# Optimization experiments

Hardware: AMD Instinct MI355X
Metric: run time of the kernel (lower is better)

Reference implementation:

```python
import jax, jax.numpy as jnp
import numpy as np

V = 50000

def _spmm(edge_vals, edge_row, edge_col, x):
    # sparse (V,V) @ dense (V,F) via gather + segment_sum
    return jax.ops.segment_sum(edge_vals[:, None] * x[edge_col], edge_row, num_segments=V)

def setup_inputs() -> dict:
    key = jax.random.key(0)
    ks = jax.random.split(key, 6)
    B, Cin, Cout, K, E = 4, 128, 128, 4, 800000
    x = jax.random.normal(ks[0], (B, Cin, V), dtype=jnp.float32)
    edge_row = jax.random.randint(ks[1], (E,), 0, V, dtype=jnp.int32)
    edge_col = jax.random.randint(ks[2], (E,), 0, V, dtype=jnp.int32)
    edge_vals = jax.random.normal(ks[3], (E,), dtype=jnp.float32) * 0.05
    std = np.sqrt(2.0 / (Cin * K)).astype(np.float32)
    weights = jax.random.normal(ks[4], (K, Cin, Cout), dtype=jnp.float32) * std
    biases = jnp.full((Cout,), 0.01, dtype=jnp.float32)
    return {"x": x, "edge_row": edge_row, "edge_col": edge_col,
            "edge_vals": edge_vals, "weights": weights, "biases": biases}

def reference(x, edge_row, edge_col, edge_vals, weights, biases):
    B, Cin, Vv = x.shape
    K = weights.shape[0]
    # (B,Cin,V) -> (V, B*Cin)
    x0 = jnp.transpose(x, (2, 0, 1)).reshape(Vv, B * Cin)
    xs = [x0]
    if K > 1:
        x1 = _spmm(edge_vals, edge_row, edge_col, x0)
        xs.append(x1)
        for _ in range(2, K):
            x2 = 2.0 * _spmm(edge_vals, edge_row, edge_col, x1) - x0
            xs.append(x2)
            x0, x1 = x1, x2
    xk = jnp.stack(xs, 0).reshape(K, Vv, B, Cin)
    # tensordot over (K, Cin): (K,V,B,Cin) x (K,Cin,Cout) -> (V,B,Cout)
    out = jnp.einsum('kvbc,kco->vbo', xk, weights)
    out = out + biases
    # permute (V,B,Cout) -> (B,Cout,V)
    return jnp.transpose(out, (1, 2, 0))
```

## Files before the change

### kernel.cpp

```cpp
#include <hip/hip_runtime.h>

#define V_N   50000
#define B_N   4
#define C_IN  128
#define C_OUT 128
#define E_N   800000
#define F_N   512
#define M_TOT 200000

#define SCAN_BLK  1024
#define SCAN_NB   ((V_N + SCAN_BLK - 1) / SCAN_BLK)

typedef unsigned short ushort_t;
typedef __attribute__((ext_vector_type(8))) short short8;
typedef __attribute__((ext_vector_type(4))) float f32x4;

#define AS1 __attribute__((address_space(1)))
#define AS3 __attribute__((address_space(3)))
__device__ __forceinline__ void gl_lds16(const void* gp, void* lp) {
    __builtin_amdgcn_global_load_lds((const AS1 unsigned int*)gp,
                                     (AS3 unsigned int*)lp, 16, 0, 0);
}

__device__ __forceinline__ float bf_lo(unsigned u) { return __uint_as_float(u << 16); }
__device__ __forceinline__ float bf_hi(unsigned u) { return __uint_as_float(u & 0xFFFF0000u); }
__device__ __forceinline__ ushort_t f2bf(float f) {
    unsigned u = __float_as_uint(f);
    u += 0x7FFFu + ((u >> 16) & 1u);
    return (ushort_t)(u >> 16);
}

__global__ __launch_bounds__(256) void k_transpose_in(const float* __restrict__ x,
                                                      ushort_t* __restrict__ x0) {
    __shared__ float tile[32][33];
    int vb = blockIdx.x * 32;
    int fb = blockIdx.y * 32;
    int tx = threadIdx.x, ty = threadIdx.y;
#pragma unroll
    for (int i = 0; i < 32; i += 8) {
        int f = fb + ty + i, v = vb + tx;
        float val = 0.f;
        if (v < V_N) val = x[(size_t)f * V_N + v];
        tile[ty + i][tx] = val;
    }
    __syncthreads();
#pragma unroll
    for (int i = 0; i < 32; i += 8) {
        int v = vb + ty + i, f = fb + tx;
        if (v < V_N) x0[(size_t)v * F_N + f] = f2bf(tile[tx][ty + i]);
    }
}

__global__ __launch_bounds__(256) void k_hist(const int* __restrict__ row,
                                              int* __restrict__ counts) {
    int e = blockIdx.x * blockDim.x + threadIdx.x;
    if (e < E_N) atomicAdd(&counts[row[e]], 1);
}

__global__ __launch_bounds__(256) void k_scan_blk(const int* __restrict__ counts,
                                                  int* __restrict__ row_ptr,
                                                  int* __restrict__ blk_sums) {
    __shared__ int s[256];
    int t = threadIdx.x;
    int base = blockIdx.x * SCAN_BLK + t * 4;
    int c0 = (base + 0 < V_N) ? counts[base + 0] : 0;
    int c1 = (base + 1 < V_N) ? counts[base + 1] : 0;
    int c2 = (base + 2 < V_N) ? counts[base + 2] : 0;
    int c3 = (base + 3 < V_N) ? counts[base + 3] : 0;
    int p1 = c0, p2 = c0 + c1, p3 = c0 + c1 + c2, tot = p3 + c3;
    s[t] = tot;
    __syncthreads();
#pragma unroll
    for (int off = 1; off < 256; off <<= 1) {
        int v = (t >= off) ? s[t - off] : 0;
        __syncthreads();
        s[t] += v;
        __syncthreads();
    }
    int excl = (t == 0) ? 0 : s[t - 1];
    if (base + 0 < V_N) row_ptr[base + 0] = excl;
    if (base + 1 < V_N) row_ptr[base + 1] = excl + p1;
    if (base + 2 < V_N) row_ptr[base + 2] = excl + p2;
    if (base + 3 < V_N) row_ptr[base + 3] = excl + p3;
    if (t == 255) blk_sums[blockIdx.x] = s[255];
}

__global__ __launch_bounds__(64) void k_scan_top(const int* __restrict__ blk_sums,
                                                 int* __restrict__ blk_off) {
    int t = threadIdx.x;
    int v = (t < SCAN_NB) ? blk_sums[t] : 0;
#pragma unroll
    for (int off = 1; off < 64; off <<= 1) {
        int u = __shfl_up(v, off);
        if (t >= off) v += u;
    }
    blk_off[t] = v;
}

__global__ __launch_bounds__(256) void k_scan_add(const int* __restrict__ blk_off,
                                                  int* __restrict__ row_ptr,
                                                  int* __restrict__ next) {
    int b = blockIdx.x, t = threadIdx.x;
    int off = (b == 0) ? 0 : blk_off[b - 1];
    int base = b * SCAN_BLK + t * 4;
#pragma unroll
    for (int i = 0; i < 4; i++) {
        int idx = base + i;
        if (idx < V_N) {
            int rv = row_ptr[idx] + off;
            row_ptr[idx] = rv;
            next[idx]    = rv;
        }
    }
    if (b == 0 && t == 0) row_ptr[V_N] = blk_off[SCAN_NB - 1];
}

__global__ __launch_bounds__(256) void k_scatter(const int* __restrict__ row,
                                                 const int* __restrict__ col,
                                                 const float* __restrict__ vals,
                                                 int* __restrict__ next,
                                                 int2* __restrict__ edges) {
    int e = blockIdx.x * blockDim.x + threadIdx.x;
    if (e < E_N) {
        int r = row[e];
        int pos = atomicAdd(&next[r], 1);
        edges[pos] = make_int2(col[e], __float_as_int(vals[e]));
    }
}

__global__ __launch_bounds__(256) void k_wprep(const float* __restrict__ W,
                                               ushort_t* __restrict__ Wt) {
    int i = blockIdx.x * 256 + threadIdx.x;
    int k = i >> 14, c = (i >> 7) & 127, o = i & 127;
    Wt[((size_t)k * 128 + o) * 128 + c] = f2bf(W[i]);
}

__global__ __launch_bounds__(256) void k_spmm_bf16(const int* __restrict__ row_ptr,
                                                   const int2* __restrict__ edges,
                                                   const ushort_t* __restrict__ src,
                                                   const ushort_t* __restrict__ prev,
                                                   ushort_t* __restrict__ dst,
                                                   float alpha, float beta,
                                                   int has_prev) {
    int lane = threadIdx.x & 63;
    int g = blockIdx.x * 4 + (threadIdx.x >> 6);
    int r = g >> 1;
    int h = g & 1;
    int e0 = row_ptr[r], e1 = row_ptr[r + 1];
    float a0 = 0.f, a1 = 0.f, a2 = 0.f, a3 = 0.f;
    const ushort_t* sp = src + h * 256 + lane * 4;

    int e = e0;
    for (; e + 4 <= e1; e += 4) {
        int2 E0 = edges[e], E1 = edges[e + 1], E2 = edges[e + 2], E3 = edges[e + 3];
        uint2 g0 = *(const uint2*)(sp + (size_t)E0.x * F_N);
        uint2 g1 = *(const uint2*)(sp + (size_t)E1.x * F_N);
        uint2 g2 = *(const uint2*)(sp + (size_t)E2.x * F_N);
        uint2 g3 = *(const uint2*)(sp + (size_t)E3.x * F_N);
        float w0 = __int_as_float(E0.y), w1 = __int_as_float(E1.y);
        float w2 = __int_as_float(E2.y), w3 = __int_as_float(E3.y);
        a0 += w0 * bf_lo(g0.x); a1 += w0 * bf_hi(g0.x);
        a2 += w0 * bf_lo(g0.y); a3 += w0 * bf_hi(g0.y);
        a0 += w1 * bf_lo(g1.x); a1 += w1 * bf_hi(g1.x);
        a2 += w1 * bf_lo(g1.y); a3 += w1 * bf_hi(g1.y);
        a0 += w2 * bf_lo(g2.x); a1 += w2 * bf_hi(g2.x);
        a2 += w2 * bf_lo(g2.y); a3 += w2 * bf_hi(g2.y);
        a0 += w3 * bf_lo(g3.x); a1 += w3 * bf_hi(g3.x);
        a2 += w3 * bf_lo(g3.y); a3 += w3 * bf_hi(g3.y);
    }
    for (; e < e1; e++) {
        int2 E = edges[e];
        uint2 gv = *(const uint2*)(sp + (size_t)E.x * F_N);
        float w = __int_as_float(E.y);
        a0 += w * bf_lo(gv.x); a1 += w * bf_hi(gv.x);
        a2 += w * bf_lo(gv.y); a3 += w * bf_hi(gv.y);
    }

    size_t off = (size_t)r * F_N + h * 256 + lane * 4;
    if (has_prev) {
        uint2 pv = *(const uint2*)(prev + off);
        a0 = alpha * a0 + beta * bf_lo(pv.x);
        a1 = alpha * a1 + beta * bf_hi(pv.x);
        a2 = alpha * a2 + beta * bf_lo(pv.y);
        a3 = alpha * a3 + beta * bf_hi(pv.y);
    } else {
        a0 *= alpha; a1 *= alpha; a2 *= alpha; a3 *= alpha;
    }
    ushort_t res[4] = {f2bf(a0), f2bf(a1), f2bf(a2), f2bf(a3)};
    *(uint2*)(dst + off) = *(const uint2*)res;
}

__global__ __launch_bounds__(256, 2) void k_gemm_mfma(
        const ushort_t* __restrict__ X0, const ushort_t* __restrict__ X1,
        const ushort_t* __restrict__ X2, const ushort_t* __restrict__ X3,
        const ushort_t* __restrict__ Wt, const float* __restrict__ bias,
        float* __restrict__ out) {
    __shared__ ushort_t As[128][64];
    __shared__ ushort_t Bs[128][64];
    __shared__ float    Cs[64][133];

    int tid  = threadIdx.x;
    int lane = tid & 63;
    int wv   = tid >> 6;
    int wm = wv >> 1, wn = wv & 1;
    int quad = lane >> 4, l15 = lane & 15;
    int m_blk = blockIdx.x * 128;

    f32x4 acc[4][4];
#pragma unroll
    for (int fi = 0; fi < 4; fi++)
#pragma unroll
        for (int fj = 0; fj < 4; fj++) {
            acc[fi][fj][0] = 0.f; acc[fi][fj][1] = 0.f;
            acc[fi][fj][2] = 0.f; acc[fi][fj][3] = 0.f;
        }

    const ushort_t* Xb[4] = {X0, X1, X2, X3};

    int rr_s = lane >> 3;
    int pl   = lane & 7;
    for (int kb = 0; kb < 4; kb++) {
        const ushort_t* A = Xb[kb];
        const ushort_t* W = Wt + (size_t)kb * (128 * 128);
        for (int kk = 0; kk < 128; kk += 64) {
            __syncthreads();
#pragma unroll
            for (int i = 0; i < 4; i++) {
                int r0 = (wv * 4 + i) * 8;
                int rr = r0 + rr_s;
                int pg = pl ^ (rr & 7);
                int gm = m_blk + rr; if (gm >= M_TOT) gm = M_TOT - 1;
                gl_lds16(&A[(size_t)gm * 128 + kk + pg * 8], &As[r0][0]);
                gl_lds16(&W[(size_t)rr * 128 + kk + pg * 8], &Bs[r0][0]);
            }
            __syncthreads();

            short8 a[2][4], b[2][4];
#pragma unroll
            for (int h = 0; h < 2; h++)
#pragma unroll
                for (int f = 0; f < 4; f++) {
                    int ra = wm * 64 + f * 16 + l15;
                    int ca = (h * 4 + quad) ^ (ra & 7);
                    a[h][f] = *(const short8*)&As[ra][ca * 8];
                    int rb = wn * 64 + f * 16 + l15;
                    int cb = (h * 4 + quad) ^ (rb & 7);
                    b[h][f] = *(const short8*)&Bs[rb][cb * 8];
                }
#pragma unroll
            for (int h = 0; h < 2; h++)
#pragma unroll
                for (int fi = 0; fi < 4; fi++)
#pragma unroll
                    for (int fj = 0; fj < 4; fj++)
                        acc[fi][fj] = __builtin_amdgcn_mfma_f32_16x16x32_bf16(
                            a[h][fi], b[h][fj], acc[fi][fj], 0, 0, 0);
        }
    }

    int v_blk = m_blk >> 2;
    for (int h = 0; h < 2; h++) {
        __syncthreads();
        if (wm == h) {
#pragma unroll
            for (int fi = 0; fi < 4; fi++)
#pragma unroll
                for (int fj = 0; fj < 4; fj++) {
                    int ml = fi * 16 + quad * 4;
                    int n  = wn * 64 + fj * 16 + l15;
#pragma unroll
                    for (int reg = 0; reg < 4; reg++)
                        Cs[ml + reg][n] = acc[fi][fj][reg];
                }
        }
        __syncthreads();
#pragma unroll
        for (int i = 0; i < 8; i++) {
            int idx = tid + i * 256;
            int v4  = idx & 3;
            int o   = (idx >> 2) & 127;
            int b   = idx >> 9;
            int vl  = v4 * 4;
            float bv = bias[o];
            float r0 = Cs[(vl + 0) * 4 + b][o] + bv;
            float r1 = Cs[(vl + 1) * 4 + b][o] + bv;
            float r2 = Cs[(vl + 2) * 4 + b][o] + bv;
            float r3 = Cs[(vl + 3) * 4 + b][o] + bv;
            int v0 = v_blk + h * 16 + vl;
            float* op = out + ((size_t)b * C_OUT + o) * V_N + v0;
            if (v0 + 3 < V_N) {
                *(float4*)op = make_float4(r0, r1, r2, r3);
            } else {
                if (v0     < V_N) op[0] = r0;
                if (v0 + 1 < V_N) op[1] = r1;
                if (v0 + 2 < V_N) op[2] = r2;
                if (v0 + 3 < V_N) op[3] = r3;
            }
        }
    }
}

extern "C" void kernel_launch(void* const* d_in, const int* in_sizes, int n_in,
                              void* d_out, int out_size, void* d_ws, size_t ws_size,
                              hipStream_t stream) {
    const float* x        = (const float*)d_in[0];
    const int*   edge_row = (const int*)  d_in[1];
    const int*   edge_col = (const int*)  d_in[2];
    const float* edge_val = (const float*)d_in[3];
    const float* weights  = (const float*)d_in[4];
    const float* biases   = (const float*)d_in[5];
    float* out = (float*)d_out;

    const size_t XSZ = (size_t)V_N * F_N;
    ushort_t* x0 = (ushort_t*)d_ws;
    ushort_t* x1 = x0 + XSZ;
    ushort_t* x2 = x1 + XSZ;
    ushort_t* x3 = x2 + XSZ;
    ushort_t* Wt = x3 + XSZ;
    int* iw      = (int*)(Wt + 4 * 128 * 128);
    int* row_ptr = iw;
    int* counts  = iw + 50016;
    int* nxt     = iw + 100032;
    int* blk_sums= iw + 150048;
    int* blk_off = iw + 150112;
    int2* edges  = (int2*)(iw + 150176);

    dim3 tb(32, 8);
    dim3 tgrid((V_N + 31) / 32, F_N / 32);

    k_transpose_in<<<tgrid, tb, 0, stream>>>(x, x0);

    hipMemsetAsync(counts, 0, V_N * sizeof(int), stream);
    k_hist<<<(E_N + 255) / 256, 256, 0, stream>>>(edge_row, counts);
    k_scan_blk<<<SCAN_NB, 256, 0, stream>>>(counts, row_ptr, blk_sums);
    k_scan_top<<<1, 64, 0, stream>>>(blk_sums, blk_off);
    k_scan_add<<<SCAN_NB, 256, 0, stream>>>(blk_off, row_ptr, nxt);
    k_scatter<<<(E_N + 255) / 256, 256, 0, stream>>>(edge_row, edge_col, edge_val,
                                                     nxt, edges);

    k_wprep<<<256, 256, 0, stream>>>(weights, Wt);

    k_spmm_bf16<<<V_N * 2 / 4, 256, 0, stream>>>(row_ptr, edges, x0, x0, x1,
                                                 1.f, 0.f, 0);
    k_spmm_bf16<<<V_N * 2 / 4, 256, 0, stream>>>(row_ptr, edges, x1, x0, x2,
                                                 2.f, -1.f, 1);
    k_spmm_bf16<<<V_N * 2 / 4, 256, 0, stream>>>(row_ptr, edges, x2, x1, x3,
                                                 2.f, -1.f, 1);

    k_gemm_mfma<<<(M_TOT + 127) / 128, 256, 0, stream>>>(x0, x1, x2, x3, Wt,
                                                         biases, out);
}
```

Baseline: 698.9 us.

## Fold Chebyshev recurrence into weights and vectorize input transpose

Rewrites the Chebyshev basis in terms of plain powers of the sparse matrix, folding the recurrence coefficients into the preprocessed weight tensor so each SpMM no longer reads the previous term or applies alpha/beta. The input transpose kernel is also widened to 128-vertex tiles with float4 loads and 4-element bf16 stores. This removes a dense read per SpMM and improves transpose coalescing, at the cost of different bf16 rounding behaviour since powers are stored instead of Chebyshev terms.

After: 687.6 us. About the same (-1.6%).

```diff
diff --git a/kernel.cpp b/kernel.cpp
--- a/kernel.cpp
+++ b/kernel.cpp
@@ -32,22 +32,43 @@
 
 __global__ __launch_bounds__(256) void k_transpose_in(const float* __restrict__ x,
                                                       ushort_t* __restrict__ x0) {
-    __shared__ float tile[32][33];
-    int vb = blockIdx.x * 32;
+    __shared__ float tile[32][133];
+    int vb = blockIdx.x * 128;
     int fb = blockIdx.y * 32;
-    int tx = threadIdx.x, ty = threadIdx.y;
-#pragma unroll
-    for (int i = 0; i < 32; i += 8) {
-        int f = fb + ty + i, v = vb + tx;
-        float val = 0.f;
-        if (v < V_N) val = x[(size_t)f * V_N + v];
-        tile[ty + i][tx] = val;
+    int tid = threadIdx.x;
+    int fo = tid >> 5;
+    int vo = (tid & 31) * 4;
+#pragma unroll
+    for (int p = 0; p < 4; p++) {
+        int f = fb + fo + p * 8;
+        int v = vb + vo;
+        float4 val = make_float4(0.f, 0.f, 0.f, 0.f);
+        const float* xp = &x[(size_t)f * V_N + v];
+        if (v + 3 < V_N) {
+            val = *(const float4*)xp;
+        } else {
+            if (v     < V_N) val.x = xp[0];
+            if (v + 1 < V_N) val.y = xp[1];
+            if (v + 2 < V_N) val.z = xp[2];
+            if (v + 3 < V_N) val.w = xp[3];
+        }
+        tile[fo + p * 8][vo + 0] = val.x;
+        tile[fo + p * 8][vo + 1] = val.y;
+        tile[fo + p * 8][vo + 2] = val.z;
+        tile[fo + p * 8][vo + 3] = val.w;
     }
     __syncthreads();
-#pragma unroll
-    for (int i = 0; i < 32; i += 8) {
-        int v = vb + ty + i, f = fb + tx;
-        if (v < V_N) x0[(size_t)v * F_N + f] = f2bf(tile[tx][ty + i]);
+    int fl = (tid & 7) * 4;
+    int vbase = tid >> 3;
+#pragma unroll
+    for (int i = 0; i < 4; i++) {
+        int vloc = vbase + i * 32;
+        int v = vb + vloc;
+        if (v < V_N) {
+            ushort_t r[4] = { f2bf(tile[fl + 0][vloc]), f2bf(tile[fl + 1][vloc]),
+                              f2bf(tile[fl + 2][vloc]), f2bf(tile[fl + 3][vloc]) };
+            *(uint2*)&x0[(size_t)v * F_N + fb + fl] = *(const uint2*)r;
+        }
     }
 }
 
@@ -131,17 +152,21 @@
 __global__ __launch_bounds__(256) void k_wprep(const float* __restrict__ W,
                                                ushort_t* __restrict__ Wt) {
     int i = blockIdx.x * 256 + threadIdx.x;
-    int k = i >> 14, c = (i >> 7) & 127, o = i & 127;
-    Wt[((size_t)k * 128 + o) * 128 + c] = f2bf(W[i]);
+    int c = i >> 7, o = i & 127;
+    float w0 = W[0 * 16384 + c * 128 + o];
+    float w1 = W[1 * 16384 + c * 128 + o];
+    float w2 = W[2 * 16384 + c * 128 + o];
+    float w3 = W[3 * 16384 + c * 128 + o];
+    Wt[((size_t)0 * 128 + o) * 128 + c] = f2bf(w0 - w2);
+    Wt[((size_t)1 * 128 + o) * 128 + c] = f2bf(w1 - 3.f * w3);
+    Wt[((size_t)2 * 128 + o) * 128 + c] = f2bf(2.f * w2);
+    Wt[((size_t)3 * 128 + o) * 128 + c] = f2bf(4.f * w3);
 }
 
 __global__ __launch_bounds__(256) void k_spmm_bf16(const int* __restrict__ row_ptr,
                                                    const int2* __restrict__ edges,
                                                    const ushort_t* __restrict__ src,
-                                                   const ushort_t* __restrict__ prev,
-                                                   ushort_t* __restrict__ dst,
-                                                   float alpha, float beta,
-                                                   int has_prev) {
+                                                   ushort_t* __restrict__ dst) {
     int lane = threadIdx.x & 63;
     int g = blockIdx.x * 4 + (threadIdx.x >> 6);
     int r = g >> 1;
@@ -177,15 +202,6 @@
     }
 
     size_t off = (size_t)r * F_N + h * 256 + lane * 4;
-    if (has_prev) {
-        uint2 pv = *(const uint2*)(prev + off);
-        a0 = alpha * a0 + beta * bf_lo(pv.x);
-        a1 = alpha * a1 + beta * bf_hi(pv.x);
-        a2 = alpha * a2 + beta * bf_lo(pv.y);
-        a3 = alpha * a3 + beta * bf_hi(pv.y);
-    } else {
-        a0 *= alpha; a1 *= alpha; a2 *= alpha; a3 *= alpha;
-    }
     ushort_t res[4] = {f2bf(a0), f2bf(a1), f2bf(a2), f2bf(a3)};
     *(uint2*)(dst + off) = *(const uint2*)res;
 }
@@ -325,10 +341,8 @@
     int* blk_off = iw + 150112;
     int2* edges  = (int2*)(iw + 150176);
 
-    dim3 tb(32, 8);
-    dim3 tgrid((V_N + 31) / 32, F_N / 32);
-
-    k_transpose_in<<<tgrid, tb, 0, stream>>>(x, x0);
+    dim3 tgrid((V_N + 127) / 128, F_N / 32);
+    k_transpose_in<<<tgrid, 256, 0, stream>>>(x, x0);
 
     hipMemsetAsync(counts, 0, V_N * sizeof(int), stream);
     k_hist<<<(E_N + 255) / 256, 256, 0, stream>>>(edge_row, counts);
@@ -338,14 +352,11 @@
     k_scatter<<<(E_N + 255) / 256, 256, 0, stream>>>(edge_row, edge_col, edge_val,
                                                      nxt, edges);
 
-    k_wprep<<<256, 256, 0, stream>>>(weights, Wt);
-
-    k_spmm_bf16<<<V_N * 2 / 4, 256, 0, stream>>>(row_ptr, edges, x0, x0, x1,
-                                                 1.f, 0.f, 0);
-    k_spmm_bf16<<<V_N * 2 / 4, 256, 0, stream>>>(row_ptr, edges, x1, x0, x2,
-                                                 2.f, -1.f, 1);
-    k_spmm_bf16<<<V_N * 2 / 4, 256, 0, stream>>>(row_ptr, edges, x2, x1, x3,
-                                                 2.f, -1.f, 1);
+    k_wprep<<<64, 256, 0, stream>>>(weights, Wt);
+
+    k_spmm_bf16<<<V_N * 2 / 4, 256, 0, stream>>>(row_ptr, edges, x0, x1);
+    k_spmm_bf16<<<V_N * 2 / 4, 256, 0, stream>>>(row_ptr, edges, x1, x2);
+    k_spmm_bf16<<<V_N * 2 / 4, 256, 0, stream>>>(row_ptr, edges, x2, x3);
 
     k_gemm_mfma<<<(M_TOT + 127) / 128, 256, 0, stream>>>(x0, x1, x2, x3, Wt,
                                                          biases, out);
```
